# Kernel tuning notes

Hardware: AMD Instinct MI355X
Metric: run time of the kernel (lower is better)

The kernel has to match this reference:

```python
import jax, jax.numpy as jnp
import numpy as np
import math

B, S, HID, NH = 2, 2048, 1024, 16
HD = HID // NH  # head_dim = 64
TEMPERATURE = 1.0


def setup_inputs() -> dict:
    key = jax.random.key(0)
    ks = jax.random.split(key, 6)
    w = lambda k: (jax.random.normal(k, (HID, HID), dtype=jnp.float32) * 0.02)
    return {
        "hidden_states": jax.random.normal(ks[0], (B, S, HID), dtype=jnp.float32),
        "attention_mask": jnp.ones((B, S), dtype=jnp.float32),
        "Wq": w(ks[1]), "bq": jnp.zeros((HID,), jnp.float32),
        "Wk": w(ks[2]), "bk": jnp.zeros((HID,), jnp.float32),
        "Wv": w(ks[3]), "bv": jnp.zeros((HID,), jnp.float32),
        "Wo": w(ks[4]), "bo": jnp.zeros((HID,), jnp.float32),
    }


def reference(hidden_states, attention_mask, Wq, bq, Wk, bk, Wv, bv, Wo, bo):
    b, s, hid = hidden_states.shape
    heads = lambda x: x.reshape(b, s, NH, HD).transpose(0, 2, 1, 3)  # [b,h,s,d]

    q = heads(hidden_states @ Wq.T + bq)
    k = heads(hidden_states @ Wk.T + bk)
    v = heads(hidden_states @ Wv.T + bv)

    # padding mask applied multiplicatively to k and v
    m = attention_mask[:, None, :, None]  # [b,1,s,1]
    k = k * m
    v = v * m

    # auxiliary Hopfield state: k^T @ v per head -> [b,h,d,d]
    state = jnp.einsum("bhsd,bhse->bhde", k, v)

    # energy / scores
    energy = jnp.einsum("bhqd,bhkd->bhqk", q, k) / (TEMPERATURE * math.sqrt(HD))
    causal = jnp.triu(jnp.ones((s, s), dtype=bool), k=1)  # True above diagonal
    energy = jnp.where(causal[None, None], -jnp.inf, energy)
    energy = jnp.where(attention_mask[:, None, None, :] == 0, -jnp.inf, energy)

    attn = jax.nn.softmax(energy, axis=-1)
    out = jnp.einsum("bhqk,bhkd->bhqd", attn, v)
    out = out.transpose(0, 2, 1, 3).reshape(b, s, hid)
    out = out @ Wo.T + bo
    return out, state
```

## Files before the change

kernel.cpp:

```cpp
#include <hip/hip_runtime.h>
#include <hip/hip_bf16.h>

#define B_ 2
#define S_ 2048
#define HID_ 1024
#define NH_ 16
#define HD_ 64
#define MTOK (B_*S_)
#define LDQKV 3072

typedef __attribute__((ext_vector_type(8))) __bf16 bf16x8;
typedef __attribute__((ext_vector_type(4))) __bf16 bf16x4;
typedef __attribute__((ext_vector_type(4))) float f32x4;

__device__ __forceinline__ void gl16(__bf16* lds, const __bf16* g) {
  __builtin_amdgcn_global_load_lds(
      (const __attribute__((address_space(1))) void*)g,
      (__attribute__((address_space(3))) void*)lds, 16, 0, 0);
}

__device__ __forceinline__ int gswz(int row) { return ((row ^ (row >> 2)) & 3) << 4; }

__global__ __launch_bounds__(256) void cast_all(
    const float* __restrict__ X,
    const float* __restrict__ Wq, const float* __restrict__ Wk,
    const float* __restrict__ Wv, const float* __restrict__ Wo,
    __bf16* __restrict__ Xb, __bf16* __restrict__ Wqkvb, __bf16* __restrict__ Wob)
{
  int i = blockIdx.x * 256 + threadIdx.x;
  const float* src; __bf16* dst; int j;
  if (i < (1 << 20))              { src = X;  dst = Xb;                 j = i; }
  else if (i < (1<<20)+(1<<18))   { src = Wq; dst = Wqkvb;              j = i - (1<<20); }
  else if (i < (1<<20)+(2<<18))   { src = Wk; dst = Wqkvb + (1<<20);    j = i - (1<<20) - (1<<18); }
  else if (i < (1<<20)+(3<<18))   { src = Wv; dst = Wqkvb + (2<<20);    j = i - (1<<20) - (2<<18); }
  else                            { src = Wo; dst = Wob;                j = i - (1<<20) - (3<<18); }
  float4 v = reinterpret_cast<const float4*>(src)[j];
  bf16x4 o;
  o[0] = (__bf16)v.x; o[1] = (__bf16)v.y; o[2] = (__bf16)v.z; o[3] = (__bf16)v.w;
  reinterpret_cast<bf16x4*>(dst)[j] = o;
}

__global__ __launch_bounds__(256) void gemm_qkv(
    const __bf16* __restrict__ A, const __bf16* __restrict__ W,
    const float* __restrict__ bq, const float* __restrict__ bk,
    const float* __restrict__ bv, const float* __restrict__ mask,
    __bf16* __restrict__ C)
{
  __shared__ __bf16 SM[24576];
  const int t = threadIdx.x;
  const int m0 = blockIdx.y * 128;
  const int n0 = blockIdx.x * 128;
  const int lane = t & 63;
  const int w = t >> 6;
  const int wr = (w >> 1) * 64;
  const int wc = (w & 1) * 64;
  const int fr = lane & 15;
  const int kg = lane >> 4;

  f32x4 acc[4][4];
  #pragma unroll
  for (int i = 0; i < 4; i++)
    #pragma unroll
    for (int j = 0; j < 4; j++) acc[i][j] = (f32x4)0.f;

  const int srow = w * 16 + (lane >> 2);
  const int scolb = ((lane & 3) * 16) ^ gswz(srow);
  const __bf16* ap0 = A + (size_t)(m0 + srow) * HID_ + (scolb >> 1);
  const __bf16* ap1 = A + (size_t)(m0 + 64 + srow) * HID_ + (scolb >> 1);
  const __bf16* wp0 = W + (size_t)(n0 + srow) * HID_ + (scolb >> 1);
  const __bf16* wp1 = W + (size_t)(n0 + 64 + srow) * HID_ + (scolb >> 1);

  #define STAGE3(buf, koff) { \
    __bf16* ab = SM + (buf) * 4096; \
    __bf16* bb = SM + 12288 + (buf) * 4096; \
    gl16(ab + w * 512, ap0 + (koff)); \
    gl16(ab + 2048 + w * 512, ap1 + (koff)); \
    gl16(bb + w * 512, wp0 + (koff)); \
    gl16(bb + 2048 + w * 512, wp1 + (koff)); }

  STAGE3(0, 0);
  STAGE3(1, 32);
  int bc = 0, bp2 = 2;
  for (int step = 0; step < 32; ++step) {
    if (step + 1 < 32) { asm volatile("s_waitcnt vmcnt(4)" ::: "memory"); }
    else               { asm volatile("s_waitcnt vmcnt(0)" ::: "memory"); }
    __builtin_amdgcn_sched_barrier(0);
    __builtin_amdgcn_s_barrier();
    if (step + 2 < 32) STAGE3(bp2, (step + 2) * 32);

    const __bf16* ab = SM + bc * 4096;
    const __bf16* bb = SM + 12288 + bc * 4096;
    bf16x8 af[4], bf[4];
    #pragma unroll
    for (int m = 0; m < 4; m++) {
      int row = wr + m*16 + fr;
      af[m] = *(const bf16x8*)((const char*)ab + row * 64 + ((kg * 16) ^ gswz(row)));
    }
    #pragma unroll
    for (int n = 0; n < 4; n++) {
      int row = wc + n*16 + fr;
      bf[n] = *(const bf16x8*)((const char*)bb + row * 64 + ((kg * 16) ^ gswz(row)));
    }
    #pragma unroll
    for (int m = 0; m < 4; m++)
      #pragma unroll
      for (int n = 0; n < 4; n++)
        acc[m][n] = __builtin_amdgcn_mfma_f32_16x16x32_bf16(af[m], bf[n], acc[m][n], 0, 0, 0);

    bc = (bc == 2) ? 0 : bc + 1;
    bp2 = (bp2 == 2) ? 0 : bp2 + 1;
  }

  const int region = n0 >> 10;
  const float* bias = region == 0 ? bq : (region == 1 ? bk : bv);
  const int nloc = n0 & 1023;

  #pragma unroll
  for (int m = 0; m < 4; m++) {
    #pragma unroll
    for (int r = 0; r < 4; r++) {
      int row = m0 + wr + m*16 + kg*4 + r;
      float rs = region ? mask[row] : 1.f;
      #pragma unroll
      for (int n = 0; n < 4; n++) {
        int c = wc + n*16 + fr;
        C[(size_t)row * LDQKV + n0 + c] = (__bf16)((acc[m][n][r] + bias[nloc + c]) * rs);
      }
    }
  }
}

__global__ __launch_bounds__(256) void transpose_kv(
    const __bf16* __restrict__ Kin, const __bf16* __restrict__ Vin,
    __bf16* __restrict__ Kt, __bf16* __restrict__ Vt)
{
  __shared__ __bf16 tile[64][68];
  const int tok0 = blockIdx.x * 64;
  const int f0 = blockIdx.y * 64;
  const __bf16* in = blockIdx.z ? Vin : Kin;
  __bf16* out = blockIdx.z ? Vt : Kt;
  const int t = threadIdx.x;
  const int r = t >> 2;
  const int c0 = (t & 3) * 16;
  const __bf16* src = in + (size_t)(tok0 + r) * LDQKV + f0 + c0;
  *(bf16x8*)&tile[r][c0]     = *(const bf16x8*)src;
  *(bf16x8*)&tile[r][c0 + 8] = *(const bf16x8*)(src + 8);
  __syncthreads();
  bf16x8 o0, o1;
  #pragma unroll
  for (int j = 0; j < 8; j++) { o0[j] = tile[c0 + j][r]; o1[j] = tile[c0 + 8 + j][r]; }
  __bf16* dst = out + (size_t)(f0 + r) * MTOK + tok0 + c0;
  *(bf16x8*)dst = o0;
  *(bf16x8*)(dst + 8) = o1;
}

__global__ __launch_bounds__(256) void gemm_o(
    const __bf16* __restrict__ A, const __bf16* __restrict__ W,
    const float* __restrict__ bias, const float* __restrict__ part,
    float* __restrict__ C)
{
  if (blockIdx.y >= 32) {
    const int bl = blockIdx.x + (blockIdx.y - 32) * 8;
    const int tid = bl * 256 + threadIdx.x;
    float* outState = C + (size_t)MTOK * HID_;
    #pragma unroll 4
    for (int e = 0; e < 32; e++) {
      int i = e * 4096 + tid;
      int bh = i >> 12, de = i & 4095;
      float s = 0.f;
      #pragma unroll
      for (int sc = 0; sc < 8; sc++) s += part[(size_t)((bh << 3) + sc) * 4096 + de];
      outState[i] = s;
    }
    return;
  }

  __shared__ __bf16 SM[24576];
  const int t = threadIdx.x;
  const int m0 = blockIdx.y * 128;
  const int n0 = blockIdx.x * 128;
  const int lane = t & 63;
  const int w = t >> 6;
  const int wr = (w >> 1) * 64;
  const int wc = (w & 1) * 64;
  const int fr = lane & 15;
  const int kg = lane >> 4;

  f32x4 acc[4][4];
  #pragma unroll
  for (int i = 0; i < 4; i++)
    #pragma unroll
    for (int j = 0; j < 4; j++) acc[i][j] = (f32x4)0.f;

  const int srow = w * 16 + (lane >> 2);
  const int scolb = ((lane & 3) * 16) ^ gswz(srow);
  const __bf16* ap0 = A + (size_t)(m0 + srow) * HID_ + (scolb >> 1);
  const __bf16* ap1 = A + (size_t)(m0 + 64 + srow) * HID_ + (scolb >> 1);
  const __bf16* wp0 = W + (size_t)(n0 + srow) * HID_ + (scolb >> 1);
  const __bf16* wp1 = W + (size_t)(n0 + 64 + srow) * HID_ + (scolb >> 1);

  STAGE3(0, 0);
  STAGE3(1, 32);
  int bc = 0, bp2 = 2;
  for (int step = 0; step < 32; ++step) {
    if (step + 1 < 32) { asm volatile("s_waitcnt vmcnt(4)" ::: "memory"); }
    else               { asm volatile("s_waitcnt vmcnt(0)" ::: "memory"); }
    __builtin_amdgcn_sched_barrier(0);
    __builtin_amdgcn_s_barrier();
    if (step + 2 < 32) STAGE3(bp2, (step + 2) * 32);

    const __bf16* ab = SM + bc * 4096;
    const __bf16* bb = SM + 12288 + bc * 4096;
    bf16x8 af[4], bf[4];
    #pragma unroll
    for (int m = 0; m < 4; m++) {
      int row = wr + m*16 + fr;
      af[m] = *(const bf16x8*)((const char*)ab + row * 64 + ((kg * 16) ^ gswz(row)));
    }
    #pragma unroll
    for (int n = 0; n < 4; n++) {
      int row = wc + n*16 + fr;
      bf[n] = *(const bf16x8*)((const char*)bb + row * 64 + ((kg * 16) ^ gswz(row)));
    }
    #pragma unroll
    for (int m = 0; m < 4; m++)
      #pragma unroll
      for (int n = 0; n < 4; n++)
        acc[m][n] = __builtin_amdgcn_mfma_f32_16x16x32_bf16(af[m], bf[n], acc[m][n], 0, 0, 0);

    bc = (bc == 2) ? 0 : bc + 1;
    bp2 = (bp2 == 2) ? 0 : bp2 + 1;
  }

  #pragma unroll
  for (int m = 0; m < 4; m++) {
    #pragma unroll
    for (int r = 0; r < 4; r++) {
      int row = m0 + wr + m*16 + kg*4 + r;
      #pragma unroll
      for (int n = 0; n < 4; n++) {
        int col = n0 + wc + n*16 + fr;
        C[(size_t)row * HID_ + col] = acc[m][n][r] + bias[col];
      }
    }
  }
}

#define SCALE_LOG2E 0.18033688011112043f

__device__ __forceinline__ bf16x8 ld_swz(const __bf16* base, int row, int xb) {
  return *(const bf16x8*)((const char*)base + row * 128 + (xb ^ ((row & 7) << 4)));
}
__device__ __forceinline__ void st_swz16(__bf16* base, int row, int colbyte, __bf16 v) {
  *(__bf16*)((char*)base + row * 128 + (colbyte ^ ((row & 7) << 4))) = v;
}
__device__ __forceinline__ bf16x8 ld_swz256(const __bf16* base, int row, int xb) {
  return *(const bf16x8*)((const char*)base + row * 256 + (xb ^ ((row & 7) << 4)));
}

__device__ __forceinline__ void attn_tile(
    const __bf16* __restrict__ ks, const __bf16* __restrict__ vs,
    const bool (&okm)[4], __bf16* __restrict__ pw,
    const bf16x8 (&qa)[2], f32x4 (&acc)[4], f32x4& accl,
    const bf16x8 ones, int q0w, int kt, int fc, int kg)
{
  f32x4 s[4];
  #pragma unroll
  for (int n = 0; n < 4; n++) s[n] = (f32x4)0.f;
  __builtin_amdgcn_s_setprio(1);
  #pragma unroll
  for (int kd = 0; kd < 2; kd++)
    #pragma unroll
    for (int n = 0; n < 4; n++) {
      bf16x8 kf = ld_swz(ks, n * 16 + fc, kd * 64 + kg * 16);
      s[n] = __builtin_amdgcn_mfma_f32_16x16x32_bf16(qa[kd], kf, s[n], 0, 0, 0);
    }
  __builtin_amdgcn_s_setprio(0);

  const int g4 = kg * 4;
  const bool fullt = (kt * 64 + 63 <= q0w);
  if (fullt) {
    #pragma unroll
    for (int r = 0; r < 4; r++)
      #pragma unroll
      for (int n = 0; n < 4; n++) {
        float p = okm[n] ? __builtin_amdgcn_exp2f(s[n][r] * SCALE_LOG2E) : 0.f;
        st_swz16(pw, g4 + r, (n * 16 + fc) * 2, (__bf16)p);
      }
  } else {
    #pragma unroll
    for (int r = 0; r < 4; r++) {
      const int qg = q0w + g4 + r;
      #pragma unroll
      for (int n = 0; n < 4; n++) {
        bool ok = okm[n] && (kt * 64 + n * 16 + fc <= qg);
        float p = ok ? __builtin_amdgcn_exp2f(s[n][r] * SCALE_LOG2E) : 0.f;
        st_swz16(pw, g4 + r, (n * 16 + fc) * 2, (__bf16)p);
      }
    }
  }

  __builtin_amdgcn_s_setprio(1);
  #pragma unroll
  for (int kc = 0; kc < 2; kc++) {
    bf16x8 pf = ld_swz(pw, fc, kc * 64 + kg * 16);
    accl = __builtin_amdgcn_mfma_f32_16x16x32_bf16(pf, ones, accl, 0, 0, 0);
    #pragma unroll
    for (int n = 0; n < 4; n++) {
      bf16x8 vf = ld_swz(vs, n * 16 + fc, kc * 64 + kg * 16);
      acc[n] = __builtin_amdgcn_mfma_f32_16x16x32_bf16(pf, vf, acc[n], 0, 0, 0);
    }
  }
  __builtin_amdgcn_s_setprio(0);
}

__global__ __launch_bounds__(256) void flash_mfma(
    const __bf16* __restrict__ Q, const __bf16* __restrict__ K,
    const __bf16* __restrict__ Vt, const float* __restrict__ mask,
    __bf16* __restrict__ O)
{
  __shared__ __bf16 Ks[2][64 * 64];
  __shared__ __bf16 Vs[2][64 * 64];
  __shared__ __bf16 Ps[4][16 * 64];

  const int bh = blockIdx.x;
  const int qt = 31 - (int)blockIdx.y;
  const int b = bh >> 4, h = bh & 15;
  const int t = threadIdx.x;
  const int w = t >> 6;
  const int lane = t & 63;
  const int fc = lane & 15;
  const int kg = lane >> 4;
  const int g4 = kg * 4;

  const int q0w = qt * 64 + w * 16;
  const size_t tokbase = (size_t)b * S_;

  const int rr = lane >> 3;
  const int cswz = ((lane & 7) ^ rr) * 8;
  const int ktmax = qt;

  bf16x8 qa[2];
  {
    const __bf16* qp = Q + (tokbase + q0w + fc) * LDQKV + h * HD_;
    qa[0] = *(const bf16x8*)(qp + kg * 8);
    qa[1] = *(const bf16x8*)(qp + 32 + kg * 8);
  }

  const float* mp = mask + tokbase + fc;
  float mnxt[4];
  #pragma unroll
  for (int n = 0; n < 4; n++) mnxt[n] = mp[n * 16];

  const __bf16* kp0 = K + (tokbase + (size_t)(w * 16 + rr)) * LDQKV + h * HD_ + cswz;
  const __bf16* kp1 = kp0 + (size_t)8 * LDQKV;
  const __bf16* vp0 = Vt + (size_t)(h * HD_ + w * 16 + rr) * MTOK + tokbase + cswz;
  const __bf16* vp1 = vp0 + (size_t)8 * MTOK;

  gl16(&Ks[0][(w * 16) * 64],     kp0);
  gl16(&Ks[0][(w * 16 + 8) * 64], kp1);
  gl16(&Vs[0][(w * 16) * 64],     vp0);
  gl16(&Vs[0][(w * 16 + 8) * 64], vp1);
  kp0 += (size_t)64 * LDQKV; kp1 += (size_t)64 * LDQKV;
  vp0 += 64; vp1 += 64;

  bf16x8 ones;
  #pragma unroll
  for (int j = 0; j < 8; j++) ones[j] = (__bf16)1.f;

  f32x4 acc[4], accl;
  #pragma unroll
  for (int n = 0; n < 4; n++) acc[n] = (f32x4)0.f;
  accl = (f32x4)0.f;

  __bf16* pw = &Ps[w][0];

  for (int kt = 0; kt <= ktmax; ++kt) {
    const int cur = kt & 1;
    float mcur[4];
    #pragma unroll
    for (int n = 0; n < 4; n++) mcur[n] = mnxt[n];

    if (kt < ktmax) {
      #pragma unroll
      for (int n = 0; n < 4; n++) mnxt[n] = mp[(kt + 1) * 64 + n * 16];
      const int nxt = cur ^ 1;
      gl16(&Ks[nxt][(w * 16) * 64],     kp0);
      gl16(&Ks[nxt][(w * 16 + 8) * 64], kp1);
      gl16(&Vs[nxt][(w * 16) * 64],     vp0);
      gl16(&Vs[nxt][(w * 16 + 8) * 64], vp1);
      kp0 += (size_t)64 * LDQKV; kp1 += (size_t)64 * LDQKV;
      vp0 += 64; vp1 += 64;
      asm volatile("s_waitcnt vmcnt(8)" ::: "memory");
    } else {
      asm volatile("s_waitcnt vmcnt(0)" ::: "memory");
    }
    __builtin_amdgcn_sched_barrier(0);
    __builtin_amdgcn_s_barrier();

    bool okm[4];
    #pragma unroll
    for (int n = 0; n < 4; n++) okm[n] = (mcur[n] != 0.f);

    attn_tile(&Ks[cur][0], &Vs[cur][0], okm, pw, qa, acc, accl, ones, q0w, kt, fc, kg);

    __builtin_amdgcn_s_barrier();
  }

  #pragma unroll
  for (int r = 0; r < 4; r++) {
    float inv = accl[r] > 0.f ? 1.f / accl[r] : 0.f;
    __bf16* op = O + (tokbase + q0w + g4 + r) * HID_ + h * HD_;
    #pragma unroll
    for (int n = 0; n < 4; n++)
      op[n * 16 + fc] = (__bf16)(acc[n][r] * inv);
  }
}

__global__ __launch_bounds__(256) void state_mfma(
    const __bf16* __restrict__ Kt, const __bf16* __restrict__ Vt,
    float* __restrict__ part)
{
  __shared__ __bf16 Kl[64 * 128];
  __shared__ __bf16 Vl[64 * 128];
  const int bh = blockIdx.x, sc = blockIdx.y;
  const int b = bh >> 4, h = bh & 15;
  const int t = threadIdx.x;
  const int w = t >> 6;
  const int lane = t & 63;
  const int fc = lane & 15;
  const int kg = lane >> 4;
  const int rloc = lane >> 4;
  const int cb = (lane & 15) * 16;

  f32x4 acc[4];
  #pragma unroll
  for (int n = 0; n < 4; n++) acc[n] = (f32x4)0.f;

  for (int ch = 0; ch < 2; ch++) {
    const size_t colbase = (size_t)b * S_ + sc * 256 + ch * 128;
    __syncthreads();
    #pragma unroll
    for (int c = 0; c < 4; c++) {
      int row = w * 16 + c * 4 + rloc;
      int scol = (cb ^ ((row & 7) << 4)) >> 1;
      gl16(&Kl[(w * 16 + c * 4) * 128], Kt + (size_t)(h * HD_ + row) * MTOK + colbase + scol);
      gl16(&Vl[(w * 16 + c * 4) * 128], Vt + (size_t)(h * HD_ + row) * MTOK + colbase + scol);
    }
    __syncthreads();

    #pragma unroll
    for (int ks = 0; ks < 4; ks++) {
      bf16x8 af = ld_swz256(Kl, w * 16 + fc, ks * 64 + kg * 16);
      #pragma unroll
      for (int n = 0; n < 4; n++) {
        bf16x8 bfr = ld_swz256(Vl, n * 16 + fc, ks * 64 + kg * 16);
        acc[n] = __builtin_amdgcn_mfma_f32_16x16x32_bf16(af, bfr, acc[n], 0, 0, 0);
      }
    }
  }

  float* dst = part + ((size_t)((bh << 3) + sc) << 12);
  #pragma unroll
  for (int n = 0; n < 4; n++)
    #pragma unroll
    for (int r = 0; r < 4; r++)
      dst[(w * 16 + kg * 4 + r) * 64 + n * 16 + fc] = acc[n][r];
}

extern "C" void kernel_launch(void* const* d_in, const int* in_sizes, int n_in,
                              void* d_out, int out_size, void* d_ws, size_t ws_size,
                              hipStream_t stream)
{
  const float* hs   = (const float*)d_in[0];
  const float* mask = (const float*)d_in[1];
  const float* Wq   = (const float*)d_in[2];
  const float* bq   = (const float*)d_in[3];
  const float* Wk   = (const float*)d_in[4];
  const float* bk   = (const float*)d_in[5];
  const float* Wv   = (const float*)d_in[6];
  const float* bv   = (const float*)d_in[7];
  const float* Wo   = (const float*)d_in[8];
  const float* bo   = (const float*)d_in[9];
  float* out = (float*)d_out;

  char* ws = (char*)d_ws;
  __bf16* Wqkvb = (__bf16*)(ws);
  __bf16* Wob   = (__bf16*)(ws + (6u  << 20));
  __bf16* Xb    = (__bf16*)(ws + (8u  << 20));
  __bf16* QKV   = (__bf16*)(ws + (16u << 20));
  __bf16* Ob    = (__bf16*)(ws + (40u << 20));
  __bf16* Ktg   = (__bf16*)(ws + (48u << 20));

  cast_all<<<8192, 256, 0, stream>>>(hs, Wq, Wk, Wv, Wo, Xb, Wqkvb, Wob);

  gemm_qkv<<<dim3(LDQKV / 128, MTOK / 128), 256, 0, stream>>>(
      Xb, Wqkvb, bq, bk, bv, mask, QKV);

  __bf16* Vtg = Xb;
  transpose_kv<<<dim3(MTOK / 64, HID_ / 64, 2), 256, 0, stream>>>(
      QKV + 1024, QKV + 2048, Ktg, Vtg);

  flash_mfma<<<dim3(B_ * NH_, 32), 256, 0, stream>>>(
      QKV, QKV + 1024, Vtg, mask, Ob);

  float* part = (float*)Wqkvb;
  state_mfma<<<dim3(B_ * NH_, 8), 256, 0, stream>>>(Ktg, Vtg, part);

  gemm_o<<<dim3(HID_ / 128, 34), 256, 0, stream>>>(Ob, Wob, bo, part, out);
}
```

Before: 126.3 us.

## Process two query tiles per attention block and fold softmax scale into Q

```diff
diff --git a/kernel.cpp b/kernel.cpp
--- a/kernel.cpp
+++ b/kernel.cpp
@@ -8,6 +8,7 @@
 #define HD_ 64
 #define MTOK (B_*S_)
 #define LDQKV 3072
+#define SCALE_LOG2E 0.18033688011112043f
 
 typedef __attribute__((ext_vector_type(8))) __bf16 bf16x8;
 typedef __attribute__((ext_vector_type(4))) __bf16 bf16x4;
@@ -120,7 +121,7 @@
     #pragma unroll
     for (int r = 0; r < 4; r++) {
       int row = m0 + wr + m*16 + kg*4 + r;
-      float rs = region ? mask[row] : 1.f;
+      float rs = region ? mask[row] : SCALE_LOG2E;
       #pragma unroll
       for (int n = 0; n < 4; n++) {
         int c = wc + n*16 + fr;
@@ -246,8 +247,6 @@
   }
 }
 
-#define SCALE_LOG2E 0.18033688011112043f
-
 __device__ __forceinline__ bf16x8 ld_swz(const __bf16* base, int row, int xb) {
   return *(const bf16x8*)((const char*)base + row * 128 + (xb ^ ((row & 7) << 4)));
 }
@@ -258,25 +257,10 @@
   return *(const bf16x8*)((const char*)base + row * 256 + (xb ^ ((row & 7) << 4)));
 }
 
-__device__ __forceinline__ void attn_tile(
-    const __bf16* __restrict__ ks, const __bf16* __restrict__ vs,
-    const bool (&okm)[4], __bf16* __restrict__ pw,
-    const bf16x8 (&qa)[2], f32x4 (&acc)[4], f32x4& accl,
-    const bf16x8 ones, int q0w, int kt, int fc, int kg)
-{
-  f32x4 s[4];
-  #pragma unroll
-  for (int n = 0; n < 4; n++) s[n] = (f32x4)0.f;
-  __builtin_amdgcn_s_setprio(1);
-  #pragma unroll
-  for (int kd = 0; kd < 2; kd++)
-    #pragma unroll
-    for (int n = 0; n < 4; n++) {
-      bf16x8 kf = ld_swz(ks, n * 16 + fc, kd * 64 + kg * 16);
-      s[n] = __builtin_amdgcn_mfma_f32_16x16x32_bf16(qa[kd], kf, s[n], 0, 0, 0);
-    }
-  __builtin_amdgcn_s_setprio(0);
-
+__device__ __forceinline__ void softmax_store(
+    const f32x4 (&s)[4], __bf16* __restrict__ pw,
+    const bool (&okm)[4], int q0w, int kt, int fc, int kg)
+{
   const int g4 = kg * 4;
   const bool fullt = (kt * 64 + 63 <= q0w);
   if (fullt) {
@@ -284,7 +268,7 @@
     for (int r = 0; r < 4; r++)
       #pragma unroll
       for (int n = 0; n < 4; n++) {
-        float p = okm[n] ? __builtin_amdgcn_exp2f(s[n][r] * SCALE_LOG2E) : 0.f;
+        float p = okm[n] ? __builtin_amdgcn_exp2f(s[n][r]) : 0.f;
         st_swz16(pw, g4 + r, (n * 16 + fc) * 2, (__bf16)p);
       }
   } else {
@@ -294,24 +278,11 @@
       #pragma unroll
       for (int n = 0; n < 4; n++) {
         bool ok = okm[n] && (kt * 64 + n * 16 + fc <= qg);
-        float p = ok ? __builtin_amdgcn_exp2f(s[n][r] * SCALE_LOG2E) : 0.f;
+        float p = ok ? __builtin_amdgcn_exp2f(s[n][r]) : 0.f;
         st_swz16(pw, g4 + r, (n * 16 + fc) * 2, (__bf16)p);
       }
     }
   }
-
-  __builtin_amdgcn_s_setprio(1);
-  #pragma unroll
-  for (int kc = 0; kc < 2; kc++) {
-    bf16x8 pf = ld_swz(pw, fc, kc * 64 + kg * 16);
-    accl = __builtin_amdgcn_mfma_f32_16x16x32_bf16(pf, ones, accl, 0, 0, 0);
-    #pragma unroll
-    for (int n = 0; n < 4; n++) {
-      bf16x8 vf = ld_swz(vs, n * 16 + fc, kc * 64 + kg * 16);
-      acc[n] = __builtin_amdgcn_mfma_f32_16x16x32_bf16(pf, vf, acc[n], 0, 0, 0);
-    }
-  }
-  __builtin_amdgcn_s_setprio(0);
 }
 
 __global__ __launch_bounds__(256) void flash_mfma(
@@ -321,10 +292,11 @@
 {
   __shared__ __bf16 Ks[2][64 * 64];
   __shared__ __bf16 Vs[2][64 * 64];
-  __shared__ __bf16 Ps[4][16 * 64];
+  __shared__ __bf16 Ps[8][16 * 64];
 
   const int bh = blockIdx.x;
-  const int qt = 31 - (int)blockIdx.y;
+  const int p = 15 - (int)blockIdx.y;
+  const int qtA = 2 * p, qtB = 2 * p + 1;
   const int b = bh >> 4, h = bh & 15;
   const int t = threadIdx.x;
   const int w = t >> 6;
@@ -333,18 +305,22 @@
   const int kg = lane >> 4;
   const int g4 = kg * 4;
 
-  const int q0w = qt * 64 + w * 16;
+  const int q0A = qtA * 64 + w * 16;
+  const int q0B = qtB * 64 + w * 16;
   const size_t tokbase = (size_t)b * S_;
 
   const int rr = lane >> 3;
   const int cswz = ((lane & 7) ^ rr) * 8;
-  const int ktmax = qt;
-
-  bf16x8 qa[2];
+  const int ktmax = qtB;
+
+  bf16x8 qaA[2], qaB[2];
   {
-    const __bf16* qp = Q + (tokbase + q0w + fc) * LDQKV + h * HD_;
-    qa[0] = *(const bf16x8*)(qp + kg * 8);
-    qa[1] = *(const bf16x8*)(qp + 32 + kg * 8);
+    const __bf16* qp = Q + (tokbase + q0A + fc) * LDQKV + h * HD_;
+    qaA[0] = *(const bf16x8*)(qp + kg * 8);
+    qaA[1] = *(const bf16x8*)(qp + 32 + kg * 8);
+    const __bf16* qp2 = Q + (tokbase + q0B + fc) * LDQKV + h * HD_;
+    qaB[0] = *(const bf16x8*)(qp2 + kg * 8);
+    qaB[1] = *(const bf16x8*)(qp2 + 32 + kg * 8);
   }
 
   const float* mp = mask + tokbase + fc;
@@ -368,12 +344,13 @@
   #pragma unroll
   for (int j = 0; j < 8; j++) ones[j] = (__bf16)1.f;
 
-  f32x4 acc[4], accl;
-  #pragma unroll
-  for (int n = 0; n < 4; n++) acc[n] = (f32x4)0.f;
-  accl = (f32x4)0.f;
-
-  __bf16* pw = &Ps[w][0];
+  f32x4 accA[4], acclA, accB[4], acclB;
+  #pragma unroll
+  for (int n = 0; n < 4; n++) { accA[n] = (f32x4)0.f; accB[n] = (f32x4)0.f; }
+  acclA = (f32x4)0.f; acclB = (f32x4)0.f;
+
+  __bf16* pwA = &Ps[w * 2][0];
+  __bf16* pwB = &Ps[w * 2 + 1][0];
 
   for (int kt = 0; kt <= ktmax; ++kt) {
     const int cur = kt & 1;
@@ -398,22 +375,63 @@
     __builtin_amdgcn_sched_barrier(0);
     __builtin_amdgcn_s_barrier();
 
+    const __bf16* ks = &Ks[cur][0];
+    const __bf16* vs = &Vs[cur][0];
+    const bool actA = (kt <= qtA);
     bool okm[4];
     #pragma unroll
     for (int n = 0; n < 4; n++) okm[n] = (mcur[n] != 0.f);
 
-    attn_tile(&Ks[cur][0], &Vs[cur][0], okm, pw, qa, acc, accl, ones, q0w, kt, fc, kg);
+    f32x4 sA[4], sB[4];
+    #pragma unroll
+    for (int n = 0; n < 4; n++) { sA[n] = (f32x4)0.f; sB[n] = (f32x4)0.f; }
+    __builtin_amdgcn_s_setprio(1);
+    #pragma unroll
+    for (int kd = 0; kd < 2; kd++)
+      #pragma unroll
+      for (int n = 0; n < 4; n++) {
+        bf16x8 kf = ld_swz(ks, n * 16 + fc, kd * 64 + kg * 16);
+        if (actA) sA[n] = __builtin_amdgcn_mfma_f32_16x16x32_bf16(qaA[kd], kf, sA[n], 0, 0, 0);
+        sB[n] = __builtin_amdgcn_mfma_f32_16x16x32_bf16(qaB[kd], kf, sB[n], 0, 0, 0);
+      }
+    __builtin_amdgcn_s_setprio(0);
+
+    if (actA) softmax_store(sA, pwA, okm, q0A, kt, fc, kg);
+    softmax_store(sB, pwB, okm, q0B, kt, fc, kg);
+
+    __builtin_amdgcn_s_setprio(1);
+    #pragma unroll
+    for (int kc = 0; kc < 2; kc++) {
+      bf16x8 pfB = ld_swz(pwB, fc, kc * 64 + kg * 16);
+      acclB = __builtin_amdgcn_mfma_f32_16x16x32_bf16(pfB, ones, acclB, 0, 0, 0);
+      bf16x8 pfA;
+      if (actA) {
+        pfA = ld_swz(pwA, fc, kc * 64 + kg * 16);
+        acclA = __builtin_amdgcn_mfma_f32_16x16x32_bf16(pfA, ones, acclA, 0, 0, 0);
+      }
+      #pragma unroll
+      for (int n = 0; n < 4; n++) {
+        bf16x8 vf = ld_swz(vs, n * 16 + fc, kc * 64 + kg * 16);
+        if (actA) accA[n] = __builtin_amdgcn_mfma_f32_16x16x32_bf16(pfA, vf, accA[n], 0, 0, 0);
+        accB[n] = __builtin_amdgcn_mfma_f32_16x16x32_bf16(pfB, vf, accB[n], 0, 0, 0);
+      }
+    }
+    __builtin_amdgcn_s_setprio(0);
 
     __builtin_amdgcn_s_barrier();
   }
 
   #pragma unroll
   for (int r = 0; r < 4; r++) {
-    float inv = accl[r] > 0.f ? 1.f / accl[r] : 0.f;
-    __bf16* op = O + (tokbase + q0w + g4 + r) * HID_ + h * HD_;
-    #pragma unroll
-    for (int n = 0; n < 4; n++)
-      op[n * 16 + fc] = (__bf16)(acc[n][r] * inv);
+    float invA = acclA[r] > 0.f ? 1.f / acclA[r] : 0.f;
+    float invB = acclB[r] > 0.f ? 1.f / acclB[r] : 0.f;
+    __bf16* opA = O + (tokbase + q0A + g4 + r) * HID_ + h * HD_;
+    __bf16* opB = O + (tokbase + q0B + g4 + r) * HID_ + h * HD_;
+    #pragma unroll
+    for (int n = 0; n < 4; n++) {
+      opA[n * 16 + fc] = (__bf16)(accA[n][r] * invA);
+      opB[n * 16 + fc] = (__bf16)(accB[n][r] * invB);
+    }
   }
 }
 
@@ -501,7 +519,7 @@
   transpose_kv<<<dim3(MTOK / 64, HID_ / 64, 2), 256, 0, stream>>>(
       QKV + 1024, QKV + 2048, Ktg, Vtg);
 
-  flash_mfma<<<dim3(B_ * NH_, 32), 256, 0, stream>>>(
+  flash_mfma<<<dim3(B_ * NH_, 16), 256, 0, stream>>>(
       QKV, QKV + 1024, Vtg, mask, Ob);
 
   float* part = (float*)Wqkvb;
```

After: 158.5 us. 25.5% more time.
